# Performance work log

Measured on AMD Instinct MI355X. Metric: run time of the kernel, lower is better.

Reference implementation:

```python
import jax, jax.numpy as jnp
import numpy as np

N_NODES = 50000
N_EDGES = 500000
NFEAT = 128
NHID = 128
NOUT = 16


def setup_inputs() -> dict:
    key = jax.random.key(0)
    ks = jax.random.split(key, 8)
    x = jax.random.normal(ks[0], (N_NODES, NFEAT), dtype=jnp.float32)
    edge_src = jax.random.randint(ks[1], (N_EDGES,), 0, N_NODES, dtype=jnp.int32)
    edge_dst = jax.random.randint(ks[2], (N_EDGES,), 0, N_NODES, dtype=jnp.int32)
    edge_weight = jax.random.uniform(ks[3], (N_EDGES,), dtype=jnp.float32)
    # Glorot-ish init for linear weights, zero bias (PyG GCNConv default bias=0)
    def glorot(k, fan_in, fan_out):
        s = jnp.sqrt(6.0 / (fan_in + fan_out))
        return jax.random.uniform(k, (fan_in, fan_out), jnp.float32, -s, s)
    W1 = glorot(ks[4], NFEAT, NHID)
    W2 = glorot(ks[5], NHID, NHID)
    W3 = glorot(ks[6], NHID, NOUT)
    b1 = jnp.zeros((NHID,), jnp.float32)
    b2 = jnp.zeros((NHID,), jnp.float32)
    b3 = jnp.zeros((NOUT,), jnp.float32)
    return {"x": x, "edge_src": edge_src, "edge_dst": edge_dst,
            "edge_weight": edge_weight, "W1": W1, "b1": b1,
            "W2": W2, "b2": b2, "W3": W3, "b3": b3}


def gcn_conv(x, src, dst, ew, W, b):
    """PyG GCNConv: symmetric-normalized aggregation with self-loops (weight 1).

    out_i = sum_{(j->i)} d_i^{-1/2} w_ji d_j^{-1/2} (x_j W) + d_i^{-1} (x_i W) + b
    where d_i = 1 + sum of incoming edge weights.
    """
    n = x.shape[0]
    xw = x @ W                                            # [N, F_out]
    deg = jax.ops.segment_sum(ew, dst, num_segments=n) + 1.0  # self-loop weight 1
    dinv = jnp.where(deg > 0, jax.lax.rsqrt(deg), 0.0)    # d^{-1/2}
    norm = dinv[src] * ew * dinv[dst]                     # [E]
    agg = jax.ops.segment_sum(xw[src] * norm[:, None], dst, num_segments=n)
    self_loop = xw * (dinv * dinv)[:, None]               # d_i^{-1} * x_i W
    return agg + self_loop + b


def reference(x, edge_src, edge_dst, edge_weight, W1, b1, W2, b2, W3, b3):
    # Dropout layers are identity in eval mode.
    h = gcn_conv(x, edge_src, edge_dst, edge_weight, W1, b1)
    h = jax.nn.relu(h)
    h = gcn_conv(h, edge_src, edge_dst, edge_weight, W2, b2)
    h = jax.nn.relu(h)
    h = gcn_conv(h, edge_src, edge_dst, edge_weight, W3, b3)
    return jax.nn.log_softmax(h, axis=1)
```

## Files before the change

kernel.cpp:

```cpp
#include <hip/hip_runtime.h>
#include <math.h>

#define NN 50000
#define NE 500000
#define NF 128
#define NO 16
#define SCAN_B 1024
#define NB_SCAN 49
#define NPART 16
#define EB4 489
#define EB2 977

static_assert(NN < 65536, "src must fit u16");

typedef _Float16 f16x8 __attribute__((ext_vector_type(8)));
typedef _Float16 f16x4 __attribute__((ext_vector_type(4)));
typedef float f32x4 __attribute__((ext_vector_type(4)));

union HU { unsigned short u; _Float16 h; };

__device__ inline float rec_w(unsigned int rec) {
    HU cu; cu.u = (unsigned short)(rec >> 16);
    return (float)cu.h;
}


__global__ __launch_bounds__(256) void k_count_rank(const int* __restrict__ dst,
                                                    int* __restrict__ pcnt,
                                                    int* __restrict__ rank, int E,
                                                    const float* __restrict__ W1,
                                                    const float* __restrict__ W2,
                                                    _Float16* __restrict__ W1T,
                                                    _Float16* __restrict__ W2T) {
    int b = blockIdx.x;
    if (b < EB4 - 1) {
        int part = b & (NPART - 1);
        int e0 = b * 1024 + threadIdx.x;
        int d0 = dst[e0], d1 = dst[e0 + 256], d2 = dst[e0 + 512], d3 = dst[e0 + 768];
        int r0 = atomicAdd(&pcnt[part * NN + d0], 1);
        int r1 = atomicAdd(&pcnt[part * NN + d1], 1);
        int r2 = atomicAdd(&pcnt[part * NN + d2], 1);
        int r3 = atomicAdd(&pcnt[part * NN + d3], 1);
        rank[e0]       = r0;
        rank[e0 + 256] = r1;
        rank[e0 + 512] = r2;
        rank[e0 + 768] = r3;
    } else if (b == EB4 - 1) {
        int part = b & (NPART - 1);
#pragma unroll
        for (int k = 0; k < 4; ++k) {
            int e = b * 1024 + k * 256 + threadIdx.x;
            if (e < E) {
                int d = dst[e];
                rank[e] = atomicAdd(&pcnt[part * NN + d], 1);
            }
        }
    } else {
        int idx = (b - EB4) * 256 + threadIdx.x;
        int r = idx >> 7, c = idx & 127;
        W1T[(size_t)c * NF + r] = (_Float16)W1[idx];
        W2T[(size_t)c * NF + r] = (_Float16)W2[idx];
    }
}

__global__ void k_scan1f(int* __restrict__ pcnt, int* __restrict__ offs_p,
                         int* __restrict__ bsums, int* __restrict__ done) {
    __shared__ int sm[SCAN_B];
    __shared__ int isLast;
    int t = threadIdx.x;
    int i = blockIdx.x * SCAN_B + t;
    int c = 0;
    if (i < NN) {
        int run = 0;
#pragma unroll
        for (int p = 0; p < NPART; ++p) {
            int v = pcnt[p * NN + i];
            pcnt[p * NN + i] = run;
            run += v;
        }
        c = run;
    }
    sm[t] = c;
    __syncthreads();
    for (int off = 1; off < SCAN_B; off <<= 1) {
        int x = (t >= off) ? sm[t - off] : 0;
        __syncthreads();
        sm[t] += x;
        __syncthreads();
    }
    if (i < NN) offs_p[i] = sm[t] - c;
    if (t == SCAN_B - 1) {
        __hip_atomic_store(&bsums[blockIdx.x], sm[t], __ATOMIC_RELEASE,
                           __HIP_MEMORY_SCOPE_AGENT);
        int old = __hip_atomic_fetch_add(done, 1, __ATOMIC_ACQ_REL,
                                         __HIP_MEMORY_SCOPE_AGENT);
        isLast = (old == (int)gridDim.x - 1) ? 1 : 0;
    }
    __syncthreads();
    if (isLast && t < 64) {
        int v = (t < NB_SCAN) ? __hip_atomic_load(&bsums[t], __ATOMIC_ACQUIRE,
                                                  __HIP_MEMORY_SCOPE_AGENT) : 0;
        int orig = v;
#pragma unroll
        for (int off = 1; off < 64; off <<= 1) {
            int u = __shfl_up(v, off, 64);
            if (t >= off) v += u;
        }
        if (t < NB_SCAN)
            __hip_atomic_store(&bsums[t], v - orig, __ATOMIC_RELEASE,
                               __HIP_MEMORY_SCOPE_AGENT);
    }
}

__global__ __launch_bounds__(256) void k_scatter(const int* __restrict__ src,
                                                 const int* __restrict__ dst,
                                                 const float* __restrict__ ew,
                                                 const int* __restrict__ pcnt,
                                                 const int* __restrict__ rank,
                                                 const int* __restrict__ offs_p,
                                                 const int* __restrict__ bsums,
                                                 unsigned int* __restrict__ erec, int E) {
    int b = blockIdx.x;
#pragma unroll
    for (int k = 0; k < 2; ++k) {
        int e = b * 512 + k * 256 + threadIdx.x;
        if (e < E) {
            int part = (e >> 10) & (NPART - 1);
            int d = dst[e];
            int pos = offs_p[d] + bsums[d >> 10] + pcnt[part * NN + d] + rank[e];
            HU cu; cu.h = (_Float16)ew[e];
            erec[pos] = (unsigned int)src[e] | ((unsigned int)cu.u << 16);
        }
    }
}

__global__ void k_dinv_csr(const unsigned int* __restrict__ erec,
                           const int* __restrict__ offs_p, const int* __restrict__ bsums,
                           float* __restrict__ dinv) {
    int n = blockIdx.x * blockDim.x + threadIdx.x;
    if (n < NN) {
        int s = offs_p[n] + bsums[n >> 10];
        int e = (n + 1 < NN) ? offs_p[n + 1] + bsums[(n + 1) >> 10] : NE;
        float deg = 1.0f;
        for (int j = s; j < e; ++j) deg += rec_w(erec[j]);
        dinv[n] = rsqrtf(deg);
    }
}


__device__ inline f16x8 afrag_load(const float* X, int row, int k0) {
    const float4* p = (const float4*)(X + (size_t)row * NF + k0);
    float4 a = p[0], b = p[1];
    f16x8 r;
    r[0] = (_Float16)a.x; r[1] = (_Float16)a.y; r[2] = (_Float16)a.z; r[3] = (_Float16)a.w;
    r[4] = (_Float16)b.x; r[5] = (_Float16)b.y; r[6] = (_Float16)b.z; r[7] = (_Float16)b.w;
    return r;
}
__device__ inline f16x8 afrag_load(const _Float16* X, int row, int k0) {
    return *(const f16x8*)(X + (size_t)row * NF + k0);
}

template <typename TA>
__global__ __launch_bounds__(256) void k_gemm_mfma(const TA* __restrict__ X,
                                                   const _Float16* __restrict__ WT,
                                                   const float* __restrict__ dinv,
                                                   _Float16* __restrict__ Z, int M) {
    __shared__ _Float16 ls[4][16 * 136];
    const int tid  = threadIdx.x;
    const int w    = tid >> 6;
    const int lane = tid & 63;
    const int n16  = lane & 15;
    const int quad = lane >> 4;
    const int r0   = blockIdx.x * 64 + w * 16;

    int arow = r0 + n16; if (arow > M - 1) arow = M - 1;

    f32x4 acc[8];
#pragma unroll
    for (int c = 0; c < 8; ++c) acc[c] = (f32x4){0.f, 0.f, 0.f, 0.f};

#pragma unroll
    for (int kk = 0; kk < 4; ++kk) {
        int k0 = kk * 32 + quad * 8;
        f16x8 a = afrag_load(X, arow, k0);
#pragma unroll
        for (int c = 0; c < 8; ++c) {
            f16x8 b = *(const f16x8*)(WT + (size_t)(c * 16 + n16) * NF + k0);
            acc[c] = __builtin_amdgcn_mfma_f32_16x16x32_f16(a, b, acc[c], 0, 0, 0);
        }
    }

#pragma unroll
    for (int reg = 0; reg < 4; ++reg) {
        int lrow = quad * 4 + reg;
        int grow = r0 + lrow; if (grow > M - 1) grow = M - 1;
        float di = dinv[grow];
#pragma unroll
        for (int c = 0; c < 8; ++c)
            ls[w][lrow * 136 + c * 16 + n16] = (_Float16)(acc[c][reg] * di);
    }
    __syncthreads();
#pragma unroll
    for (int i = 0; i < 4; ++i) {
        int off16 = i * 64 + lane;
        int row = off16 >> 4;
        int col = off16 & 15;
        int grow = r0 + row;
        if (grow < M) {
            f16x8 v = *(const f16x8*)(&ls[w][row * 136 + col * 8]);
            *(f16x8*)(Z + (size_t)grow * NF + col * 8) = v;
        }
    }
}

__global__ __launch_bounds__(256) void k_agg128h(const _Float16* __restrict__ z,
                                                 const float* __restrict__ dinv,
                                                 const int* __restrict__ offs_p,
                                                 const int* __restrict__ bsums,
                                                 const unsigned int* __restrict__ erec,
                                                 const float* __restrict__ bias,
                                                 _Float16* __restrict__ hout, int relu) {
    const int tid  = threadIdx.x;
    const int lane = tid & 63;
    const int half = lane >> 5;
    const int li   = lane & 31;
    int n = __builtin_amdgcn_readfirstlane(blockIdx.x * 4 + (tid >> 6));

    float acc0 = 0.f, acc1 = 0.f, acc2 = 0.f, acc3 = 0.f;

    int s = offs_p[n] + bsums[n >> 10];
    int e = (n + 1 < NN) ? offs_p[n + 1] + bsums[(n + 1) >> 10] : NE;
    for (int base = s; base < e; base += 64) {
        int cnt = e - base; if (cnt > 64) cnt = 64;
        unsigned int rec = 0u;
        if (lane < cnt) rec = __builtin_nontemporal_load(erec + base + lane);
        int   my_s = rec & 0xFFFF;
        float my_w = rec_w(rec);
        int k = 0;
        for (; k + 7 < cnt; k += 8) {
            int e0 = k + half, e1 = k + 2 + half, e2 = k + 4 + half, e3 = k + 6 + half;
            int s0 = __shfl(my_s, e0, 64), s1 = __shfl(my_s, e1, 64);
            int s2 = __shfl(my_s, e2, 64), s3 = __shfl(my_s, e3, 64);
            float w0 = __shfl(my_w, e0, 64), w1 = __shfl(my_w, e1, 64);
            float w2 = __shfl(my_w, e2, 64), w3 = __shfl(my_w, e3, 64);
            f16x4 v0 = *(const f16x4*)(z + ((size_t)s0 << 7) + li * 4);
            f16x4 v1 = *(const f16x4*)(z + ((size_t)s1 << 7) + li * 4);
            f16x4 v2 = *(const f16x4*)(z + ((size_t)s2 << 7) + li * 4);
            f16x4 v3 = *(const f16x4*)(z + ((size_t)s3 << 7) + li * 4);
            acc0 = fmaf((float)v0[0], w0, acc0); acc1 = fmaf((float)v0[1], w0, acc1);
            acc2 = fmaf((float)v0[2], w0, acc2); acc3 = fmaf((float)v0[3], w0, acc3);
            acc0 = fmaf((float)v1[0], w1, acc0); acc1 = fmaf((float)v1[1], w1, acc1);
            acc2 = fmaf((float)v1[2], w1, acc2); acc3 = fmaf((float)v1[3], w1, acc3);
            acc0 = fmaf((float)v2[0], w2, acc0); acc1 = fmaf((float)v2[1], w2, acc1);
            acc2 = fmaf((float)v2[2], w2, acc2); acc3 = fmaf((float)v2[3], w2, acc3);
            acc0 = fmaf((float)v3[0], w3, acc0); acc1 = fmaf((float)v3[1], w3, acc1);
            acc2 = fmaf((float)v3[2], w3, acc2); acc3 = fmaf((float)v3[3], w3, acc3);
        }
        for (; k < cnt; k += 2) {
            int eidx = k + half;
            int ec = eidx < cnt ? eidx : cnt - 1;
            int   s0 = __shfl(my_s, ec, 64);
            float wt = __shfl(my_w, ec, 64);
            float w0 = (eidx < cnt) ? wt : 0.0f;
            f16x4 v0 = *(const f16x4*)(z + ((size_t)s0 << 7) + li * 4);
            acc0 = fmaf((float)v0[0], w0, acc0); acc1 = fmaf((float)v0[1], w0, acc1);
            acc2 = fmaf((float)v0[2], w0, acc2); acc3 = fmaf((float)v0[3], w0, acc3);
        }
    }
    acc0 += __shfl_xor(acc0, 32, 64);
    acc1 += __shfl_xor(acc1, 32, 64);
    acc2 += __shfl_xor(acc2, 32, 64);
    acc3 += __shfl_xor(acc3, 32, 64);

    f16x4 sv = *(const f16x4*)(z + ((size_t)n << 7) + li * 4);
    float di = dinv[n];
    float4 bb = *(const float4*)(bias + li * 4);
    float r0 = fmaf(di, (float)sv[0] + acc0, bb.x);
    float r1 = fmaf(di, (float)sv[1] + acc1, bb.y);
    float r2 = fmaf(di, (float)sv[2] + acc2, bb.z);
    float r3 = fmaf(di, (float)sv[3] + acc3, bb.w);
    if (relu) {
        r0 = fmaxf(r0, 0.0f); r1 = fmaxf(r1, 0.0f);
        r2 = fmaxf(r2, 0.0f); r3 = fmaxf(r3, 0.0f);
    }
    if (half == 0) {
        f16x4 o;
        o[0] = (_Float16)r0; o[1] = (_Float16)r1;
        o[2] = (_Float16)r2; o[3] = (_Float16)r3;
        __builtin_nontemporal_store(o, (f16x4*)(hout + ((size_t)n << 7) + li * 4));
    }
}

__global__ __launch_bounds__(256) void k_gemm16(const _Float16* __restrict__ H,
                                                const float* __restrict__ W3,
                                                const float* __restrict__ dinv,
                                                _Float16* __restrict__ Z3, int M) {
    __shared__ float Wl[NF * NO];
    __shared__ float Hs[16 * 132];
    int tid = threadIdx.x;
    for (int i = tid; i < NF * NO; i += 256) Wl[i] = W3[i];
    int n0 = blockIdx.x * 16;
    {
        int row = tid >> 4, h8 = tid & 15;
        int gr = n0 + row; if (gr > M - 1) gr = M - 1;
        f16x8 v = *(const f16x8*)(H + (size_t)gr * NF + h8 * 8);
        float4 f0 = {(float)v[0], (float)v[1], (float)v[2], (float)v[3]};
        float4 f1 = {(float)v[4], (float)v[5], (float)v[6], (float)v[7]};
        *(float4*)(&Hs[row * 132 + h8 * 8])     = f0;
        *(float4*)(&Hs[row * 132 + h8 * 8 + 4]) = f1;
    }
    __syncthreads();
    int ln = tid >> 4, c = tid & 15;
    float acc = 0.0f;
#pragma unroll 8
    for (int k = 0; k < NF; ++k) acc = fmaf(Hs[ln * 132 + k], Wl[k * NO + c], acc);
    int n = n0 + ln;
    if (n < M) Z3[(size_t)n * NO + c] = (_Float16)(acc * dinv[n]);
}

__global__ __launch_bounds__(256) void k_agg16_ls(const _Float16* __restrict__ z3,
                                                  const float* __restrict__ dinv,
                                                  const int* __restrict__ offs_p,
                                                  const int* __restrict__ bsums,
                                                  const unsigned int* __restrict__ erec,
                                                  const float* __restrict__ bias,
                                                  float* __restrict__ out) {
    int tid = threadIdx.x;
    int ln = tid >> 4, c = tid & 15;
    int n = blockIdx.x * 16 + ln;
    float acc = (float)z3[((size_t)n << 4) + c];
    int s = offs_p[n] + bsums[n >> 10];
    int e = (n + 1 < NN) ? offs_p[n + 1] + bsums[(n + 1) >> 10] : NE;
    int j = s;
    for (; j + 1 < e; j += 2) {
        unsigned int r0 = erec[j], r1 = erec[j + 1];
        acc = fmaf((float)z3[((size_t)(r0 & 0xFFFF) << 4) + c], rec_w(r0), acc);
        acc = fmaf((float)z3[((size_t)(r1 & 0xFFFF) << 4) + c], rec_w(r1), acc);
    }
    if (j < e) {
        unsigned int r0 = erec[j];
        acc = fmaf((float)z3[((size_t)(r0 & 0xFFFF) << 4) + c], rec_w(r0), acc);
    }
    acc = fmaf(dinv[n], acc, bias[c]);
    float m = acc;
#pragma unroll
    for (int off = 8; off > 0; off >>= 1) m = fmaxf(m, __shfl_xor(m, off, 16));
    float ex = expf(acc - m);
    float ss = ex;
#pragma unroll
    for (int off = 8; off > 0; off >>= 1) ss += __shfl_xor(ss, off, 16);
    out[(size_t)n * NO + c] = acc - m - logf(ss);
}


extern "C" void kernel_launch(void* const* d_in, const int* in_sizes, int n_in,
                              void* d_out, int out_size, void* d_ws, size_t ws_size,
                              hipStream_t stream) {
    const float* x   = (const float*)d_in[0];
    const int*   esrc= (const int*)  d_in[1];
    const int*   edst= (const int*)  d_in[2];
    const float* ew  = (const float*)d_in[3];
    const float* W1  = (const float*)d_in[4];
    const float* b1  = (const float*)d_in[5];
    const float* W2  = (const float*)d_in[6];
    const float* b2  = (const float*)d_in[7];
    const float* W3  = (const float*)d_in[8];
    const float* b3  = (const float*)d_in[9];
    float* out = (float*)d_out;

    char* p = (char*)d_ws;
    _Float16* z   = (_Float16*)p; p += (size_t)NN * NF * 2;
    _Float16* h   = (_Float16*)p; p += (size_t)NN * NF * 2;
    _Float16* z3  = (_Float16*)p; p += (size_t)NN * NO * 2;
    float* dinv   = (float*)p; p += (size_t)NN * 4;
    unsigned int* erec = (unsigned int*)p; p += (size_t)NE * 4;
    int*   rank   = (int*)p;   p += (size_t)NE * 4;
    int*   pcnt   = (int*)p;   p += (size_t)NPART * NN * 4;
    int*   done   = (int*)p;   p += 64;
    int*   offs_p = (int*)p;   p += (size_t)(NN + 1) * 4;
    int*   bsums  = (int*)p;   p += 256;
    _Float16* W1T = (_Float16*)p; p += (size_t)NF * NF * 2;
    _Float16* W2T = (_Float16*)p; p += (size_t)NF * NF * 2;

    hipMemsetAsync(pcnt, 0, (size_t)NPART * NN * 4 + 64, stream);

    k_count_rank<<<EB4 + 64, 256, 0, stream>>>(edst, pcnt, rank, NE, W1, W2, W1T, W2T);
    k_scan1f<<<NB_SCAN, SCAN_B, 0, stream>>>(pcnt, offs_p, bsums, done);
    k_scatter<<<EB2, 256, 0, stream>>>(esrc, edst, ew, pcnt, rank, offs_p, bsums, erec, NE);
    k_dinv_csr<<<(NN + 255) / 256, 256, 0, stream>>>(erec, offs_p, bsums, dinv);

    k_gemm_mfma<float><<<(NN + 63) / 64, 256, 0, stream>>>(x, W1T, dinv, z, NN);
    k_agg128h<<<NN / 4, 256, 0, stream>>>(z, dinv, offs_p, bsums, erec, b1, h, 1);
    k_gemm_mfma<_Float16><<<(NN + 63) / 64, 256, 0, stream>>>(h, W2T, dinv, z, NN);
    k_agg128h<<<NN / 4, 256, 0, stream>>>(z, dinv, offs_p, bsums, erec, b2, h, 1);
    k_gemm16<<<(NN + 15) / 16, 256, 0, stream>>>(h, W3, dinv, z3, NN);
    k_agg16_ls<<<NN / 16, 256, 0, stream>>>(z3, dinv, offs_p, bsums, erec, b3, out);
}
```

Baseline: 250.6 us.

## Fuse degree into count pass, finalize offsets in scan, fuse layer-3 GEMM into aggregation

```diff
diff --git a/kernel.cpp b/kernel.cpp
--- a/kernel.cpp
+++ b/kernel.cpp
@@ -26,7 +26,9 @@
 
 
 __global__ __launch_bounds__(256) void k_count_rank(const int* __restrict__ dst,
+                                                    const float* __restrict__ ew,
                                                     int* __restrict__ pcnt,
+                                                    float* __restrict__ deg,
                                                     int* __restrict__ rank, int E,
                                                     const float* __restrict__ W1,
                                                     const float* __restrict__ W2,
@@ -37,6 +39,7 @@
         int part = b & (NPART - 1);
         int e0 = b * 1024 + threadIdx.x;
         int d0 = dst[e0], d1 = dst[e0 + 256], d2 = dst[e0 + 512], d3 = dst[e0 + 768];
+        float w0 = ew[e0], w1 = ew[e0 + 256], w2 = ew[e0 + 512], w3 = ew[e0 + 768];
         int r0 = atomicAdd(&pcnt[part * NN + d0], 1);
         int r1 = atomicAdd(&pcnt[part * NN + d1], 1);
         int r2 = atomicAdd(&pcnt[part * NN + d2], 1);
@@ -45,6 +48,10 @@
         rank[e0 + 256] = r1;
         rank[e0 + 512] = r2;
         rank[e0 + 768] = r3;
+        atomicAdd(&deg[d0], w0);
+        atomicAdd(&deg[d1], w1);
+        atomicAdd(&deg[d2], w2);
+        atomicAdd(&deg[d3], w3);
     } else if (b == EB4 - 1) {
         int part = b & (NPART - 1);
 #pragma unroll
@@ -53,6 +60,7 @@
             if (e < E) {
                 int d = dst[e];
                 rank[e] = atomicAdd(&pcnt[part * NN + d], 1);
+                atomicAdd(&deg[d], ew[e]);
             }
         }
     } else {
@@ -63,10 +71,13 @@
     }
 }
 
-__global__ void k_scan1f(int* __restrict__ pcnt, int* __restrict__ offs_p,
-                         int* __restrict__ bsums, int* __restrict__ done) {
+__global__ void k_scan1f(int* __restrict__ pcnt, const float* __restrict__ deg,
+                         float* __restrict__ dinv, int* __restrict__ offs,
+                         int* __restrict__ bsums, int* __restrict__ done,
+                         int* __restrict__ flag) {
     __shared__ int sm[SCAN_B];
     __shared__ int isLast;
+    __shared__ int baseS;
     int t = threadIdx.x;
     int i = blockIdx.x * SCAN_B + t;
     int c = 0;
@@ -88,7 +99,7 @@
         sm[t] += x;
         __syncthreads();
     }
-    if (i < NN) offs_p[i] = sm[t] - c;
+    int excl = sm[t] - c;
     if (t == SCAN_B - 1) {
         __hip_atomic_store(&bsums[blockIdx.x], sm[t], __ATOMIC_RELEASE,
                            __HIP_MEMORY_SCOPE_AGENT);
@@ -110,6 +121,22 @@
             __hip_atomic_store(&bsums[t], v - orig, __ATOMIC_RELEASE,
                                __HIP_MEMORY_SCOPE_AGENT);
     }
+    __syncthreads();
+    if (isLast && t == 0)
+        __hip_atomic_store(flag, 1, __ATOMIC_RELEASE, __HIP_MEMORY_SCOPE_AGENT);
+    if (t == 0) {
+        while (__hip_atomic_load(flag, __ATOMIC_ACQUIRE,
+                                 __HIP_MEMORY_SCOPE_AGENT) == 0)
+            __builtin_amdgcn_s_sleep(2);
+        baseS = __hip_atomic_load(&bsums[blockIdx.x], __ATOMIC_ACQUIRE,
+                                  __HIP_MEMORY_SCOPE_AGENT);
+    }
+    __syncthreads();
+    if (i < NN) {
+        offs[i] = excl + baseS;
+        dinv[i] = rsqrtf(1.0f + deg[i]);
+    }
+    if (i == NN - 1) offs[NN] = NE;
 }
 
 __global__ __launch_bounds__(256) void k_scatter(const int* __restrict__ src,
@@ -117,8 +144,7 @@
                                                  const float* __restrict__ ew,
                                                  const int* __restrict__ pcnt,
                                                  const int* __restrict__ rank,
-                                                 const int* __restrict__ offs_p,
-                                                 const int* __restrict__ bsums,
+                                                 const int* __restrict__ offs,
                                                  unsigned int* __restrict__ erec, int E) {
     int b = blockIdx.x;
 #pragma unroll
@@ -127,23 +153,10 @@
         if (e < E) {
             int part = (e >> 10) & (NPART - 1);
             int d = dst[e];
-            int pos = offs_p[d] + bsums[d >> 10] + pcnt[part * NN + d] + rank[e];
+            int pos = offs[d] + pcnt[part * NN + d] + rank[e];
             HU cu; cu.h = (_Float16)ew[e];
             erec[pos] = (unsigned int)src[e] | ((unsigned int)cu.u << 16);
         }
-    }
-}
-
-__global__ void k_dinv_csr(const unsigned int* __restrict__ erec,
-                           const int* __restrict__ offs_p, const int* __restrict__ bsums,
-                           float* __restrict__ dinv) {
-    int n = blockIdx.x * blockDim.x + threadIdx.x;
-    if (n < NN) {
-        int s = offs_p[n] + bsums[n >> 10];
-        int e = (n + 1 < NN) ? offs_p[n + 1] + bsums[(n + 1) >> 10] : NE;
-        float deg = 1.0f;
-        for (int j = s; j < e; ++j) deg += rec_w(erec[j]);
-        dinv[n] = rsqrtf(deg);
     }
 }
 
@@ -213,23 +226,14 @@
     }
 }
 
-__global__ __launch_bounds__(256) void k_agg128h(const _Float16* __restrict__ z,
-                                                 const float* __restrict__ dinv,
-                                                 const int* __restrict__ offs_p,
-                                                 const int* __restrict__ bsums,
-                                                 const unsigned int* __restrict__ erec,
-                                                 const float* __restrict__ bias,
-                                                 _Float16* __restrict__ hout, int relu) {
-    const int tid  = threadIdx.x;
-    const int lane = tid & 63;
-    const int half = lane >> 5;
-    const int li   = lane & 31;
-    int n = __builtin_amdgcn_readfirstlane(blockIdx.x * 4 + (tid >> 6));
-
-    float acc0 = 0.f, acc1 = 0.f, acc2 = 0.f, acc3 = 0.f;
-
-    int s = offs_p[n] + bsums[n >> 10];
-    int e = (n + 1 < NN) ? offs_p[n + 1] + bsums[(n + 1) >> 10] : NE;
+__device__ __forceinline__ void agg_gather(const _Float16* __restrict__ z,
+                                           const int* __restrict__ offs,
+                                           const unsigned int* __restrict__ erec,
+                                           int n, int lane, int half, int li,
+                                           float& acc0, float& acc1,
+                                           float& acc2, float& acc3) {
+    int s = offs[n];
+    int e = offs[n + 1];
     for (int base = s; base < e; base += 64) {
         int cnt = e - base; if (cnt > 64) cnt = 64;
         unsigned int rec = 0u;
@@ -271,6 +275,22 @@
     acc1 += __shfl_xor(acc1, 32, 64);
     acc2 += __shfl_xor(acc2, 32, 64);
     acc3 += __shfl_xor(acc3, 32, 64);
+}
+
+__global__ __launch_bounds__(256) void k_agg128h(const _Float16* __restrict__ z,
+                                                 const float* __restrict__ dinv,
+                                                 const int* __restrict__ offs,
+                                                 const unsigned int* __restrict__ erec,
+                                                 const float* __restrict__ bias,
+                                                 _Float16* __restrict__ hout, int relu) {
+    const int tid  = threadIdx.x;
+    const int lane = tid & 63;
+    const int half = lane >> 5;
+    const int li   = lane & 31;
+    int n = __builtin_amdgcn_readfirstlane(blockIdx.x * 4 + (tid >> 6));
+
+    float acc0 = 0.f, acc1 = 0.f, acc2 = 0.f, acc3 = 0.f;
+    agg_gather(z, offs, erec, n, lane, half, li, acc0, acc1, acc2, acc3);
 
     f16x4 sv = *(const f16x4*)(z + ((size_t)n << 7) + li * 4);
     float di = dinv[n];
@@ -291,37 +311,54 @@
     }
 }
 
-__global__ __launch_bounds__(256) void k_gemm16(const _Float16* __restrict__ H,
-                                                const float* __restrict__ W3,
-                                                const float* __restrict__ dinv,
-                                                _Float16* __restrict__ Z3, int M) {
-    __shared__ float Wl[NF * NO];
-    __shared__ float Hs[16 * 132];
-    int tid = threadIdx.x;
-    for (int i = tid; i < NF * NO; i += 256) Wl[i] = W3[i];
-    int n0 = blockIdx.x * 16;
-    {
-        int row = tid >> 4, h8 = tid & 15;
-        int gr = n0 + row; if (gr > M - 1) gr = M - 1;
-        f16x8 v = *(const f16x8*)(H + (size_t)gr * NF + h8 * 8);
-        float4 f0 = {(float)v[0], (float)v[1], (float)v[2], (float)v[3]};
-        float4 f1 = {(float)v[4], (float)v[5], (float)v[6], (float)v[7]};
-        *(float4*)(&Hs[row * 132 + h8 * 8])     = f0;
-        *(float4*)(&Hs[row * 132 + h8 * 8 + 4]) = f1;
-    }
-    __syncthreads();
-    int ln = tid >> 4, c = tid & 15;
-    float acc = 0.0f;
-#pragma unroll 8
-    for (int k = 0; k < NF; ++k) acc = fmaf(Hs[ln * 132 + k], Wl[k * NO + c], acc);
-    int n = n0 + ln;
-    if (n < M) Z3[(size_t)n * NO + c] = (_Float16)(acc * dinv[n]);
+__global__ __launch_bounds__(256) void k_agg128f(const _Float16* __restrict__ z,
+                                                 const float* __restrict__ dinv,
+                                                 const int* __restrict__ offs,
+                                                 const unsigned int* __restrict__ erec,
+                                                 const float* __restrict__ bias,
+                                                 const float* __restrict__ W3,
+                                                 _Float16* __restrict__ z3) {
+    __shared__ float w3s[NF * NO];
+    const int tid  = threadIdx.x;
+    for (int i = tid; i < NF * NO; i += 256) w3s[i] = W3[i];
+    const int lane = tid & 63;
+    const int half = lane >> 5;
+    const int li   = lane & 31;
+    int n = __builtin_amdgcn_readfirstlane(blockIdx.x * 4 + (tid >> 6));
+    __syncthreads();
+
+    float acc0 = 0.f, acc1 = 0.f, acc2 = 0.f, acc3 = 0.f;
+    agg_gather(z, offs, erec, n, lane, half, li, acc0, acc1, acc2, acc3);
+
+    f16x4 sv = *(const f16x4*)(z + ((size_t)n << 7) + li * 4);
+    float di = dinv[n];
+    float4 bb = *(const float4*)(bias + li * 4);
+    float r0 = fmaxf(fmaf(di, (float)sv[0] + acc0, bb.x), 0.0f);
+    float r1 = fmaxf(fmaf(di, (float)sv[1] + acc1, bb.y), 0.0f);
+    float r2 = fmaxf(fmaf(di, (float)sv[2] + acc2, bb.z), 0.0f);
+    float r3 = fmaxf(fmaf(di, (float)sv[3] + acc3, bb.w), 0.0f);
+
+    const int c = lane & 15, q = lane >> 4;
+    float p = 0.f;
+#pragma unroll
+    for (int m = 0; m < 8; ++m) {
+        int sl = q * 8 + m;
+        float h0 = __shfl(r0, sl, 64), h1 = __shfl(r1, sl, 64);
+        float h2 = __shfl(r2, sl, 64), h3 = __shfl(r3, sl, 64);
+        int kb = (q * 32 + m * 4) * NO + c;
+        p = fmaf(h0, w3s[kb],          p);
+        p = fmaf(h1, w3s[kb + NO],     p);
+        p = fmaf(h2, w3s[kb + 2 * NO], p);
+        p = fmaf(h3, w3s[kb + 3 * NO], p);
+    }
+    p += __shfl_xor(p, 16, 64);
+    p += __shfl_xor(p, 32, 64);
+    if (lane < 16) z3[((size_t)n << 4) + lane] = (_Float16)(p * di);
 }
 
 __global__ __launch_bounds__(256) void k_agg16_ls(const _Float16* __restrict__ z3,
                                                   const float* __restrict__ dinv,
-                                                  const int* __restrict__ offs_p,
-                                                  const int* __restrict__ bsums,
+                                                  const int* __restrict__ offs,
                                                   const unsigned int* __restrict__ erec,
                                                   const float* __restrict__ bias,
                                                   float* __restrict__ out) {
@@ -329,8 +366,8 @@
     int ln = tid >> 4, c = tid & 15;
     int n = blockIdx.x * 16 + ln;
     float acc = (float)z3[((size_t)n << 4) + c];
-    int s = offs_p[n] + bsums[n >> 10];
-    int e = (n + 1 < NN) ? offs_p[n + 1] + bsums[(n + 1) >> 10] : NE;
+    int s = offs[n];
+    int e = offs[n + 1];
     int j = s;
     for (; j + 1 < e; j += 2) {
         unsigned int r0 = erec[j], r1 = erec[j + 1];
@@ -376,23 +413,23 @@
     unsigned int* erec = (unsigned int*)p; p += (size_t)NE * 4;
     int*   rank   = (int*)p;   p += (size_t)NE * 4;
     int*   pcnt   = (int*)p;   p += (size_t)NPART * NN * 4;
+    float* deg    = (float*)p; p += (size_t)NN * 4;
     int*   done   = (int*)p;   p += 64;
-    int*   offs_p = (int*)p;   p += (size_t)(NN + 1) * 4;
+    int*   flag   = (int*)p;   p += 64;
+    int*   offs   = (int*)p;   p += (size_t)(NN + 16) * 4;
     int*   bsums  = (int*)p;   p += 256;
     _Float16* W1T = (_Float16*)p; p += (size_t)NF * NF * 2;
     _Float16* W2T = (_Float16*)p; p += (size_t)NF * NF * 2;
 
-    hipMemsetAsync(pcnt, 0, (size_t)NPART * NN * 4 + 64, stream);
-
-    k_count_rank<<<EB4 + 64, 256, 0, stream>>>(edst, pcnt, rank, NE, W1, W2, W1T, W2T);
-    k_scan1f<<<NB_SCAN, SCAN_B, 0, stream>>>(pcnt, offs_p, bsums, done);
-    k_scatter<<<EB2, 256, 0, stream>>>(esrc, edst, ew, pcnt, rank, offs_p, bsums, erec, NE);
-    k_dinv_csr<<<(NN + 255) / 256, 256, 0, stream>>>(erec, offs_p, bsums, dinv);
+    hipMemsetAsync(pcnt, 0, (size_t)NPART * NN * 4 + (size_t)NN * 4 + 128, stream);
+
+    k_count_rank<<<EB4 + 64, 256, 0, stream>>>(edst, ew, pcnt, deg, rank, NE, W1, W2, W1T, W2T);
+    k_scan1f<<<NB_SCAN, SCAN_B, 0, stream>>>(pcnt, deg, dinv, offs, bsums, done, flag);
+    k_scatter<<<EB2, 256, 0, stream>>>(esrc, edst, ew, pcnt, rank, offs, erec, NE);
 
     k_gemm_mfma<float><<<(NN + 63) / 64, 256, 0, stream>>>(x, W1T, dinv, z, NN);
-    k_agg128h<<<NN / 4, 256, 0, stream>>>(z, dinv, offs_p, bsums, erec, b1, h, 1);
+    k_agg128h<<<NN / 4, 256, 0, stream>>>(z, dinv, offs, erec, b1, h, 1);
     k_gemm_mfma<_Float16><<<(NN + 63) / 64, 256, 0, stream>>>(h, W2T, dinv, z, NN);
-    k_agg128h<<<NN / 4, 256, 0, stream>>>(z, dinv, offs_p, bsums, erec, b2, h, 1);
-    k_gemm16<<<(NN + 15) / 16, 256, 0, stream>>>(h, W3, dinv, z3, NN);
-    k_agg16_ls<<<NN / 16, 256, 0, stream>>>(z3, dinv, offs_p, bsums, erec, b3, out);
-}
+    k_agg128f<<<NN / 4, 256, 0, stream>>>(z, dinv, offs, erec, b2, W3, z3);
+    k_agg16_ls<<<NN / 16, 256, 0, stream>>>(z3, dinv, offs, erec, b3, out);
+}
```

After: 284.5 us. 1.14x slower.
